# Kernel optimization log

Measured on AMD Instinct MI355X. Metric: run time of the kernel, lower is better.

Reference implementation:

```python
import jax, jax.numpy as jnp
import numpy as np
from jax import lax

DM = 64      # d_model
DI = 128     # d_inner = expand * d_model
DS = 16      # d_state
DC = 4       # d_conv
R = 4        # dt_rank = ceil(d_model/16)
H = 4        # num_heads
NL = 3       # num_mamba_stack
B_READS = 128
L_READ = 512
N_SEQ = 96


def setup_inputs() -> dict:
    key = jax.random.key(0)
    ks = jax.random.split(key, 20)
    f = lambda k, shape, s=0.05: jax.random.normal(k, shape, jnp.float32) * s
    A_init = jnp.broadcast_to(jnp.arange(1, DS + 1, dtype=jnp.float32), (NL, DI, DS))
    return {
        "reads": jax.random.normal(ks[0], (B_READS, L_READ, 4), jnp.float32),
        "sequenced_reads_indices": jax.random.randint(ks[1], (N_SEQ,), 0, B_READS),
        "expander_w": f(ks[2], (DM, 4), 0.3),
        "expander_b": f(ks[3], (DM,)),
        "in_proj_w": f(ks[4], (NL, 2 * DI, DM), 0.1),
        "conv_w": f(ks[5], (NL, DI, 1, DC), 0.3),
        "conv_b": f(ks[6], (NL, DI)),
        "x_proj_w": f(ks[7], (NL, R + 2 * DS, DI), 0.1),
        "dt_w": f(ks[8], (NL, DI, R), 0.3),
        "dt_b": f(ks[9], (NL, DI)),
        "A_log": jnp.log(A_init),
        "D": jnp.ones((NL, DI), jnp.float32),
        "out_w": f(ks[10], (NL, DM, DI), 0.1),
        "ln_w": jnp.ones((NL, DM), jnp.float32),
        "ln_b": jnp.zeros((NL, DM), jnp.float32),
        "query_w": f(ks[11], (DM, 2 * DM), 0.1),
        "query_b": f(ks[12], (DM,)),
        "key_w": f(ks[13], (DM, 2 * DM), 0.1),
        "key_b": f(ks[14], (DM,)),
        "mix_w": f(ks[15], (H, H), 0.3),
        "mix_b": f(ks[16], (H,)),
    }


def _mamba_block(u, in_w, cw, cb, xw, dtw, dtb, A_log, Dp, ow):
    # u: [b, l, DM]
    b, l, _ = u.shape
    xz = u @ in_w.T                              # [b, l, 2*DI]
    x, z = xz[..., :DI], xz[..., DI:]
    # causal depthwise conv along the sequence axis
    xc = lax.conv_general_dilated(
        x.transpose(0, 2, 1), cw, (1,), [(DC - 1, 0)],
        dimension_numbers=("NCH", "OIH", "NCH"), feature_group_count=DI)
    x = jax.nn.silu((xc + cb[None, :, None]).transpose(0, 2, 1))  # [b, l, DI]
    xd = x @ xw.T                                # [b, l, R + 2*DS]
    dt = jax.nn.softplus(xd[..., :R] @ dtw.T + dtb)              # [b, l, DI]
    Bm, Cm = xd[..., R:R + DS], xd[..., R + DS:]                 # [b, l, DS]
    A = -jnp.exp(A_log)                          # [DI, DS]

    def step(h, inp):
        x_t, dt_t, B_t, C_t = inp                # [b,DI],[b,DI],[b,DS],[b,DS]
        h = jnp.exp(dt_t[:, :, None] * A) * h + (dt_t * x_t)[:, :, None] * B_t[:, None, :]
        return h, jnp.einsum("bdn,bn->bd", h, C_t)

    h0 = jnp.zeros((b, DI, DS), u.dtype)
    _, ys = lax.scan(step, h0, (x.swapaxes(0, 1), dt.swapaxes(0, 1),
                                Bm.swapaxes(0, 1), Cm.swapaxes(0, 1)))
    y = ys.swapaxes(0, 1) + x * Dp               # [b, l, DI]
    y = y * jax.nn.silu(z)
    return y @ ow.T                              # [b, l, DM]


def _layer_norm(x, w, b, eps=1e-5):
    m = x.mean(-1, keepdims=True)
    v = ((x - m) ** 2).mean(-1, keepdims=True)
    return (x - m) / jnp.sqrt(v + eps) * w + b


def reference(reads, sequenced_reads_indices, expander_w, expander_b,
              in_proj_w, conv_w, conv_b, x_proj_w, dt_w, dt_b, A_log, D,
              out_w, ln_w, ln_b, query_w, query_b, key_w, key_b, mix_w, mix_b):
    h = reads @ expander_w.T + expander_b        # [b, l, DM]
    for i in range(NL):
        h = _mamba_block(h, in_proj_w[i], conv_w[i], conv_b[i], x_proj_w[i],
                         dt_w[i], dt_b[i], A_log[i], D[i], out_w[i])
        h = jax.nn.relu(_layer_norm(h, ln_w[i], ln_b[i]))
    mean_p = h.mean(1)                           # [b, DM]
    last_p = h[:, -1, :]                         # [b, DM]  (max_pooled in source is dead code)
    enc = jnp.concatenate([mean_p, last_p], axis=-1)   # [b, 2*DM]
    seq = enc[sequenced_reads_indices]                  # [q, 2*DM]
    q = (seq @ query_w.T + query_b).reshape(-1, H, DM // H).transpose(1, 0, 2)
    k = (enc @ key_w.T + key_b).reshape(-1, H, DM // H).transpose(1, 0, 2)
    scores = jnp.einsum("hqd,hkd->qkh", q, k)    # [q, b, H]
    scores = jax.nn.relu(scores) @ mix_w.T + mix_b
    return scores.max(-1)                        # [q, b]
```

## Files before the change

### kernel.cpp

```cpp
#include <hip/hip_runtime.h>
#include <hip/hip_bf16.h>
#include <math.h>

#define NLAYER 3
#define LREADx 512
#define NSEQx  96

typedef _Float16 f16x8 __attribute__((ext_vector_type(8)));
typedef _Float16 f16x4 __attribute__((ext_vector_type(4)));
typedef float    f32x4 __attribute__((ext_vector_type(4)));

__device__ __forceinline__ float fsigmoid(float v){ return 1.f/(1.f+__expf(-v)); }
__device__ __forceinline__ float fsoftplus(float v){ return fmaxf(v,0.f) + __logf(1.f + __expf(-fabsf(v))); }

__device__ __forceinline__ unsigned short f2h(float f){
  _Float16 h = (_Float16)f;
  return *reinterpret_cast<unsigned short*>(&h);
}

template<int CTRL>
__device__ __forceinline__ float dpp_add(float v){
  int x = __builtin_amdgcn_update_dpp(0, __float_as_int(v), CTRL, 0xF, 0xF, true);
  return v + __int_as_float(x);
}

__global__ __launch_bounds__(256) void k_exp(const float* __restrict__ reads,
    const float* __restrict__ ew, const float* __restrict__ eb, _Float16* __restrict__ h){
  int idx = blockIdx.x*256 + threadIdx.x;
  int dq = idx & 15;
  int row = idx >> 4;
  float4 r4 = *(const float4*)(reads + (size_t)row*4);
  f16x4 o;
  #pragma unroll
  for (int e=0;e<4;e++){
    int d = dq*4 + e;
    float4 w4 = *(const float4*)(ew + d*4);
    o[e] = (_Float16)fmaf(r4.x,w4.x, fmaf(r4.y,w4.y, fmaf(r4.z,w4.z, fmaf(r4.w,w4.w, eb[d]))));
  }
  *(f16x4*)(h + (size_t)row*64 + dq*4) = o;
}

__global__ __launch_bounds__(256) void k_wcvt(const float* __restrict__ inw,
    const float* __restrict__ ow, const float* __restrict__ xw,
    unsigned short* __restrict__ whf, unsigned short* __restrict__ owh,
    unsigned short* __restrict__ xwh){
  int i = blockIdx.x*256 + threadIdx.x;
  if (i < 49152){ whf[i] = f2h(inw[i]); return; }
  i -= 49152;
  if (i < 24576){ owh[i] = f2h(ow[i]); return; }
  i -= 24576;
  if (i < 18432){
    int l = i / 6144, rem = i % 6144;
    int r = rem >> 7, c = rem & 127;
    xwh[i] = (r < 36) ? f2h(xw[(l*36 + r)*128 + c]) : (unsigned short)0;
  }
}

__global__ __launch_bounds__(256) void k_xzc(const _Float16* __restrict__ h,
    const unsigned short* __restrict__ wb, const float* __restrict__ cw,
    const float* __restrict__ cb, _Float16* __restrict__ x, _Float16* __restrict__ zsil){
  __shared__ _Float16 hs_[80][68];
  __shared__ _Float16 xp[67][132];
  int t = threadIdx.x;
  int row0 = blockIdx.x*64;
  int l0 = row0 & 511;
  for (int i=t; i<640; i+=256){
    int r = i >> 3, q = i & 7;
    f16x8 v;
    #pragma unroll
    for (int e=0;e<8;e++) v[e] = (_Float16)0.f;
    if (!(l0==0 && r<16)) v = *(const f16x8*)(h + (size_t)(row0-16+r)*64 + q*8);
    *(f16x8*)&hs_[r][q*8] = v;
  }
  int w  = __builtin_amdgcn_readfirstlane(t >> 6);
  int ln = t & 63;
  int lr = ln & 15;
  int lk = (ln >> 4)*8;
  f16x8 bf[4][2];
  #pragma unroll
  for (int ct=0; ct<4; ct++)
    #pragma unroll
    for (int ks=0; ks<2; ks++)
      bf[ct][ks] = *(const f16x8*)(wb + (size_t)(w*64 + ct*16 + lr)*64 + ks*32 + lk);
  __syncthreads();
  f32x4 acc[5][4];
  #pragma unroll
  for (int m=0;m<5;m++)
    #pragma unroll
    for (int ct=0;ct<4;ct++) acc[m][ct] = (f32x4){0.f,0.f,0.f,0.f};
  #pragma unroll
  for (int m=0; m<5; m++){
    f16x8 a0 = *(const f16x8*)&hs_[m*16+lr][lk];
    f16x8 a1 = *(const f16x8*)&hs_[m*16+lr][32 + lk];
    #pragma unroll
    for (int ct=0; ct<4; ct++){
      acc[m][ct] = __builtin_amdgcn_mfma_f32_16x16x32_f16(a0, bf[ct][0], acc[m][ct], 0, 0, 0);
      acc[m][ct] = __builtin_amdgcn_mfma_f32_16x16x32_f16(a1, bf[ct][1], acc[m][ct], 0, 0, 0);
    }
  }
  int colb = w*64;
  #pragma unroll
  for (int m=0; m<5; m++)
    #pragma unroll
    for (int ct=0; ct<4; ct++){
      int col = colb + ct*16 + lr;
      #pragma unroll
      for (int rg=0; rg<4; rg++){
        int rl = m*16 + (ln>>4)*4 + rg;
        float v = acc[m][ct][rg];
        if (col < 128){
          if (rl >= 13) xp[rl-13][col] = (_Float16)v;
        } else {
          if (rl >= 16) zsil[(size_t)(row0 + rl - 16)*128 + (col-128)] = (_Float16)(v * fsigmoid(v));
        }
      }
    }
  __syncthreads();
  int c = t & 127, half = t >> 7;
  float4 w4 = *(const float4*)(cw + c*4);
  float bv = cb[c];
  #pragma unroll
  for (int r=half*32; r<half*32+32; r++){
    float a = fmaf((float)xp[r][c],w4.x, fmaf((float)xp[r+1][c],w4.y,
              fmaf((float)xp[r+2][c],w4.z, fmaf((float)xp[r+3][c],w4.w, bv))));
    x[(size_t)(row0+r)*128 + c] = (_Float16)(a * fsigmoid(a));
  }
}

__global__ __launch_bounds__(256) void k_xd(const _Float16* __restrict__ x,
    const unsigned short* __restrict__ xwh, const float* __restrict__ dtw,
    const float* __restrict__ dtb, float* __restrict__ dt, _Float16* __restrict__ bc){
  __shared__ _Float16 xst[64][136];
  __shared__ float xdl[64][37];
  int t = threadIdx.x;
  int row0 = blockIdx.x*64;
  for (int i=t; i<1024; i+=256){
    int r = i >> 4, q = i & 15;
    *(f16x8*)&xst[r][q*8] = *(const f16x8*)(x + (size_t)(row0+r)*128 + q*8);
  }
  __syncthreads();
  int w = __builtin_amdgcn_readfirstlane(t >> 6);
  int ln = t & 63, lr = ln & 15, kg = ln >> 4;
  f16x8 af[4];
  #pragma unroll
  for (int ks=0; ks<4; ks++) af[ks] = *(const f16x8*)&xst[w*16+lr][ks*32 + kg*8];
  f32x4 acc[3];
  #pragma unroll
  for (int ct=0;ct<3;ct++) acc[ct] = (f32x4){0.f,0.f,0.f,0.f};
  #pragma unroll
  for (int ks=0; ks<4; ks++)
    #pragma unroll
    for (int ct=0; ct<3; ct++){
      f16x8 b = *(const f16x8*)(xwh + (size_t)(ct*16 + lr)*128 + ks*32 + kg*8);
      acc[ct] = __builtin_amdgcn_mfma_f32_16x16x32_f16(af[ks], b, acc[ct], 0, 0, 0);
    }
  #pragma unroll
  for (int ct=0; ct<3; ct++){
    int c = ct*16 + lr;
    if (c < 36){
      #pragma unroll
      for (int rg=0; rg<4; rg++) xdl[w*16 + kg*4 + rg][c] = acc[ct][rg];
    }
  }
  __syncthreads();
  int d = t & 127, half = t >> 7;
  float4 w4 = *(const float4*)(dtw + d*4);
  float bv = dtb[d];
  size_t r0 = (size_t)blockIdx.x*64;
  for (int rr=half; rr<64; rr+=2){
    float v = fmaf(xdl[rr][0],w4.x, fmaf(xdl[rr][1],w4.y, fmaf(xdl[rr][2],w4.z,
              fmaf(xdl[rr][3],w4.w, bv))));
    dt[(r0+rr)*128 + d] = fsoftplus(v);
  }
  for (int i=t; i<2048; i+=256){
    int r = i >> 5, cc = i & 31;
    float vv = (cc & 1) ? xdl[r][20 + (cc>>1)] : xdl[r][4 + (cc>>1)];
    bc[(r0+r)*32 + cc] = (_Float16)vv;
  }
}

__global__ __launch_bounds__(256) void k_scan(const float* __restrict__ dt,
    const _Float16* __restrict__ x, const _Float16* __restrict__ zsil,
    const _Float16* __restrict__ bc, const float* __restrict__ alog,
    const float* __restrict__ Dp, _Float16* __restrict__ y){
  __shared__ float    dtxb[2][64*68];
  __shared__ _Float16 bcb [2][2048];
  __shared__ float    ys  [2][2048];
  int t = threadIdx.x;
  int b  = blockIdx.x & 127;
  int dg = blockIdx.x >> 7;
  int dl = t >> 3;
  int np = t & 7;
  int d  = dg*32 + dl;
  float aL1 = -__expf(alog[d*16 + 2*np])     * 1.44269504f;
  float aL2 = -__expf(alog[d*16 + 2*np + 1]) * 1.44269504f;
  float hs1 = 0.f, hs2 = 0.f;
  size_t base  = (size_t)b*512*128 + (size_t)dg*32;
  size_t baseb = (size_t)b*512*32;
  int r  = t >> 3;
  int d0 = (t & 7)*4;
  int rb = t >> 2;
  int cb_ = (t & 3)*8;
  const float*    dtA = dt   + base  + (size_t)r*128 + d0;
  const _Float16* xA  = x    + base  + (size_t)r*128 + d0;
  const _Float16* zA  = zsil + base  + (size_t)r*128 + d0;
  const _Float16* bA  = bc   + baseb + (size_t)rb*32 + cb_;
  float4 Dv4 = *(const float4*)(Dp + dg*32 + d0);

  auto stage = [&](int bsel, float4 pd0, float4 pd1, f16x4 px0, f16x4 px1, f16x8 pbh){
    float4 w0 = make_float4(pd0.x, pd0.x*(float)px0[0], pd0.y, pd0.y*(float)px0[1]);
    float4 w1 = make_float4(pd0.z, pd0.z*(float)px0[2], pd0.w, pd0.w*(float)px0[3]);
    float4 w2 = make_float4(pd1.x, pd1.x*(float)px1[0], pd1.y, pd1.y*(float)px1[1]);
    float4 w3 = make_float4(pd1.z, pd1.z*(float)px1[2], pd1.w, pd1.w*(float)px1[3]);
    *(float4*)&dtxb[bsel][r*68 + 2*d0]          = w0;
    *(float4*)&dtxb[bsel][r*68 + 2*d0 + 4]      = w1;
    *(float4*)&dtxb[bsel][(r+32)*68 + 2*d0]     = w2;
    *(float4*)&dtxb[bsel][(r+32)*68 + 2*d0 + 4] = w3;
    *(f16x8*)&bcb[bsel][rb*32 + cb_]            = pbh;
  };

  {
    float4 pd0 = *(const float4*)(dtA);
    float4 pd1 = *(const float4*)(dtA + 4096);
    f16x4  px0 = *(const f16x4*)(xA);
    f16x4  px1 = *(const f16x4*)(xA + 4096);
    f16x8  pbh = *(const f16x8*)(bA);
    stage(0, pd0, pd1, px0, px1, pbh);
  }
  asm volatile("s_waitcnt lgkmcnt(0)" ::: "memory");
  __builtin_amdgcn_s_barrier();

  for (int c=0;c<8;c++){
    int buf = c & 1;
    float4 nd0, nd1;
    f16x4  nx0, nx1;
    f16x8  nbh;
    if (c < 7){
      nd0 = *(const float4*)(dtA + (c+1)*8192);
      nd1 = *(const float4*)(dtA + (c+1)*8192 + 4096);
      nx0 = *(const f16x4*)(xA  + (c+1)*8192);
      nx1 = *(const f16x4*)(xA  + (c+1)*8192 + 4096);
      nbh = *(const f16x8*)(bA  + (c+1)*2048);
    }
    f16x4 xe0 = *(const f16x4*)(xA + c*8192);
    f16x4 xe1 = *(const f16x4*)(xA + c*8192 + 4096);
    f16x4 z0  = *(const f16x4*)(zA + c*8192);
    f16x4 z1  = *(const f16x4*)(zA + c*8192 + 4096);
    #pragma unroll 8
    for (int l=0;l<64;l++){
      float2 dx  = *(const float2*)&dtxb[buf][l*68 + 2*dl];
      f16x4 bch  = *(const f16x4*)&bcb[buf][l*32 + 4*np];
      float e1 = __builtin_amdgcn_exp2f(dx.x * aL1);
      float e2 = __builtin_amdgcn_exp2f(dx.x * aL2);
      hs1 = fmaf(e1, hs1, dx.y * (float)bch[0]);
      hs2 = fmaf(e2, hs2, dx.y * (float)bch[2]);
      float p = fmaf(hs1, (float)bch[1], hs2 * (float)bch[3]);
      p = dpp_add<0x101>(p);
      p = dpp_add<0x102>(p);
      p = dpp_add<0x104>(p);
      if (np == 0) ys[buf][l*32 + dl] = p;
    }
    if (c < 7) stage(buf^1, nd0, nd1, nx0, nx1, nbh);
    asm volatile("s_waitcnt lgkmcnt(0)" ::: "memory");
    __builtin_amdgcn_s_barrier();
    size_t yb = base + (size_t)c*8192;
    float4 s0 = *(const float4*)&ys[buf][4*t];
    float4 s1 = *(const float4*)&ys[buf][4*t + 1024];
    f16x4 o0, o1;
    o0[0] = (_Float16)((s0.x + (float)xe0[0]*Dv4.x) * (float)z0[0]);
    o0[1] = (_Float16)((s0.y + (float)xe0[1]*Dv4.y) * (float)z0[1]);
    o0[2] = (_Float16)((s0.z + (float)xe0[2]*Dv4.z) * (float)z0[2]);
    o0[3] = (_Float16)((s0.w + (float)xe0[3]*Dv4.w) * (float)z0[3]);
    o1[0] = (_Float16)((s1.x + (float)xe1[0]*Dv4.x) * (float)z1[0]);
    o1[1] = (_Float16)((s1.y + (float)xe1[1]*Dv4.y) * (float)z1[1]);
    o1[2] = (_Float16)((s1.z + (float)xe1[2]*Dv4.z) * (float)z1[2]);
    o1[3] = (_Float16)((s1.w + (float)xe1[3]*Dv4.w) * (float)z1[3]);
    *(f16x4*)(y + yb + (size_t)r*128 + d0)      = o0;
    *(f16x4*)(y + yb + (size_t)(r+32)*128 + d0) = o1;
  }
}

__global__ __launch_bounds__(256) void k_out(const _Float16* __restrict__ y,
    const unsigned short* __restrict__ owh, const float* __restrict__ lnw,
    const float* __restrict__ lnb, _Float16* __restrict__ h){
  __shared__ _Float16 yst[64][136];
  int t = threadIdx.x;
  int row0 = blockIdx.x*64;
  for (int i=t; i<1024; i+=256){
    int r = i >> 4, q = i & 15;
    *(f16x8*)&yst[r][q*8] = *(const f16x8*)(y + (size_t)(row0+r)*128 + q*8);
  }
  __syncthreads();
  int w = __builtin_amdgcn_readfirstlane(t >> 6);
  int ln = t & 63, lr = ln & 15, kg = ln >> 4;
  f16x8 af[4];
  #pragma unroll
  for (int ks=0; ks<4; ks++) af[ks] = *(const f16x8*)&yst[w*16+lr][ks*32 + kg*8];
  f32x4 acc[4];
  #pragma unroll
  for (int ct=0;ct<4;ct++) acc[ct] = (f32x4){0.f,0.f,0.f,0.f};
  #pragma unroll
  for (int ks=0; ks<4; ks++)
    #pragma unroll
    for (int ct=0; ct<4; ct++){
      f16x8 b = *(const f16x8*)(owh + (size_t)(ct*16 + lr)*128 + ks*32 + kg*8);
      acc[ct] = __builtin_amdgcn_mfma_f32_16x16x32_f16(af[ks], b, acc[ct], 0, 0, 0);
    }
  float mean[4], inv[4];
  #pragma unroll
  for (int rg=0; rg<4; rg++){
    float s = acc[0][rg] + acc[1][rg] + acc[2][rg] + acc[3][rg];
    #pragma unroll
    for (int off=1; off<16; off<<=1) s += __shfl_xor(s, off, 64);
    mean[rg] = s * (1.f/64.f);
  }
  #pragma unroll
  for (int rg=0; rg<4; rg++){
    float v = 0.f;
    #pragma unroll
    for (int ct=0; ct<4; ct++){ float dv = acc[ct][rg]-mean[rg]; v += dv*dv; }
    #pragma unroll
    for (int off=1; off<16; off<<=1) v += __shfl_xor(v, off, 64);
    inv[rg] = rsqrtf(v*(1.f/64.f) + 1e-5f);
  }
  float lw[4], lb[4];
  #pragma unroll
  for (int ct=0; ct<4; ct++){ lw[ct] = lnw[ct*16+lr]; lb[ct] = lnb[ct*16+lr]; }
  #pragma unroll
  for (int rg=0; rg<4; rg++){
    int row = row0 + w*16 + kg*4 + rg;
    #pragma unroll
    for (int ct=0; ct<4; ct++){
      float o = (acc[ct][rg]-mean[rg])*inv[rg]*lw[ct] + lb[ct];
      h[(size_t)row*64 + ct*16 + lr] = (_Float16)fmaxf(o, 0.f);
    }
  }
}

__global__ __launch_bounds__(512) void k_pool(const _Float16* __restrict__ h, float* __restrict__ enc){
  __shared__ float ps[8][64];
  int t = threadIdx.x;
  int w = t >> 6, d = t & 63;
  int b = blockIdx.x;
  const _Float16* hb = h + (size_t)b*LREADx*64;
  float s = 0.f;
  #pragma unroll 8
  for (int i=0;i<64;i++) s += (float)hb[(size_t)(w*64+i)*64 + d];
  ps[w][d] = s;
  __syncthreads();
  if (w == 0){
    float acc = 0.f;
    #pragma unroll
    for (int i=0;i<8;i++) acc += ps[i][d];
    enc[b*128 + d]      = acc * (1.f/512.f);
    enc[b*128 + 64 + d] = (float)hb[(size_t)511*64 + d];
  }
}

__global__ __launch_bounds__(256) void k_qk(const float* __restrict__ enc,
    const int* __restrict__ sidx, const float* __restrict__ qw, const float* __restrict__ qb,
    const float* __restrict__ kw, const float* __restrict__ kb,
    float* __restrict__ qbuf, float* __restrict__ kbuf){
  int idx = blockIdx.x*256 + threadIdx.x;
  if (idx < NSEQx*64){
    int qi = idx >> 6, j = idx & 63;
    const float* er = enc + (size_t)sidx[qi]*128;
    const float* wr = qw + j*128;
    float a = qb[j];
    for (int k=0;k<32;k++){
      float4 e4 = *(const float4*)(er + k*4);
      float4 w4 = *(const float4*)(wr + k*4);
      a = fmaf(e4.x,w4.x, fmaf(e4.y,w4.y, fmaf(e4.z,w4.z, fmaf(e4.w,w4.w, a))));
    }
    qbuf[idx] = a;
  } else {
    int i2 = idx - NSEQx*64;
    int ki = i2 >> 6, j = i2 & 63;
    const float* er = enc + (size_t)ki*128;
    const float* wr = kw + j*128;
    float a = kb[j];
    for (int k=0;k<32;k++){
      float4 e4 = *(const float4*)(er + k*4);
      float4 w4 = *(const float4*)(wr + k*4);
      a = fmaf(e4.x,w4.x, fmaf(e4.y,w4.y, fmaf(e4.z,w4.z, fmaf(e4.w,w4.w, a))));
    }
    kbuf[i2] = a;
  }
}

__global__ __launch_bounds__(256) void k_score(const float* __restrict__ qbuf,
    const float* __restrict__ kbuf, const float* __restrict__ mixw,
    const float* __restrict__ mixb, float* __restrict__ out){
  int idx = blockIdx.x*256 + threadIdx.x;
  int ki = idx & 127, qi = idx >> 7;
  const float* qr = qbuf + qi*64;
  const float* kr = kbuf + ki*64;
  float s[4];
  #pragma unroll
  for (int hh=0;hh<4;hh++){
    float a = 0.f;
    #pragma unroll
    for (int k=0;k<4;k++){
      float4 q4 = *(const float4*)(qr + hh*16 + k*4);
      float4 k4 = *(const float4*)(kr + hh*16 + k*4);
      a = fmaf(q4.x,k4.x, fmaf(q4.y,k4.y, fmaf(q4.z,k4.z, fmaf(q4.w,k4.w, a))));
    }
    s[hh] = fmaxf(a, 0.f);
  }
  float best = -1e30f;
  #pragma unroll
  for (int hh=0;hh<4;hh++){
    float v = mixb[hh];
    #pragma unroll
    for (int h2=0;h2<4;h2++) v = fmaf(s[h2], mixw[hh*4+h2], v);
    best = fmaxf(best, v);
  }
  out[idx] = best;
}

extern "C" void kernel_launch(void* const* d_in, const int* in_sizes, int n_in,
                              void* d_out, int out_size, void* d_ws, size_t ws_size,
                              hipStream_t stream) {
  (void)in_sizes; (void)n_in; (void)out_size; (void)ws_size;
  const float* reads = (const float*)d_in[0];
  const int*   sidx  = (const int*)d_in[1];
  const float* ew    = (const float*)d_in[2];
  const float* eb    = (const float*)d_in[3];
  const float* inw   = (const float*)d_in[4];
  const float* cw    = (const float*)d_in[5];
  const float* cb    = (const float*)d_in[6];
  const float* xw    = (const float*)d_in[7];
  const float* dtw   = (const float*)d_in[8];
  const float* dtb   = (const float*)d_in[9];
  const float* alog  = (const float*)d_in[10];
  const float* Dp    = (const float*)d_in[11];
  const float* ow    = (const float*)d_in[12];
  const float* lnw   = (const float*)d_in[13];
  const float* lnb   = (const float*)d_in[14];
  const float* qw    = (const float*)d_in[15];
  const float* qb    = (const float*)d_in[16];
  const float* kw    = (const float*)d_in[17];
  const float* kb    = (const float*)d_in[18];
  const float* mixw  = (const float*)d_in[19];
  const float* mixb  = (const float*)d_in[20];

  float* ws  = (float*)d_ws;
  _Float16* h  = (_Float16*)(ws);
  _Float16* yx = (_Float16*)(ws + 4194304);
  _Float16* zs = (_Float16*)(ws + 12582912);
  _Float16* x  = (_Float16*)(ws + 20971520);
  float* dt  = ws + 29360128;
  _Float16* bc = (_Float16*)(ws + 37748736);
  float* enc = ws + 39845888;
  float* qk  = ws + 39862272;
  unsigned short* whf = (unsigned short*)(ws + 39876608);
  unsigned short* owh = whf + 49152;
  unsigned short* xwh = owh + 24576;

  k_wcvt <<<360, 256, 0, stream>>>(inw, ow, xw, whf, owh, xwh);
  k_exp  <<<4096, 256, 0, stream>>>(reads, ew, eb, h);
  for (int l = 0; l < NLAYER; l++){
    k_xzc <<<1024, 256, 0, stream>>>(h, whf + l*16384, cw + l*512, cb + l*128, x, zs);
    k_xd  <<<1024, 256, 0, stream>>>(x, xwh + l*6144, dtw + l*512, dtb + l*128, dt, bc);
    k_scan<<<512, 256, 0, stream>>>(dt, x, zs, bc, alog + l*2048, Dp + l*128, yx);
    k_out <<<1024, 256, 0, stream>>>(yx, owh + l*8192, lnw + l*64, lnb + l*64, h);
  }
  k_pool <<<128, 512, 0, stream>>>(h, enc);
  k_qk   <<<56, 256, 0, stream>>>(enc, sidx, qw, qb, kw, kb, qk, qk + 6144);
  k_score<<<48, 256, 0, stream>>>(qk, qk + 6144, mixw, mixb, (float*)d_out);
}
```

Before: 368.0 us.

## Split scan work to one state per thread and double scan block count

The selective scan kernel now gives each thread a single state element (16 threads per channel) instead of two, and each block handles 16 channels instead of 32, so the grid doubles from 512 to 1024 blocks. The serial dependency chain per thread is halved, at the cost of one extra DPP reduction step and more blocks each re-staging the shared B/C data. Shared memory per block shrinks, which may allow higher occupancy.

```diff
diff --git a/kernel.cpp b/kernel.cpp
--- a/kernel.cpp
+++ b/kernel.cpp
@@ -8,6 +8,7 @@
 
 typedef _Float16 f16x8 __attribute__((ext_vector_type(8)));
 typedef _Float16 f16x4 __attribute__((ext_vector_type(4)));
+typedef _Float16 f16x2 __attribute__((ext_vector_type(2)));
 typedef float    f32x4 __attribute__((ext_vector_type(4)));
 
 __device__ __forceinline__ float fsigmoid(float v){ return 1.f/(1.f+__expf(-v)); }
@@ -183,100 +184,80 @@
     const _Float16* __restrict__ x, const _Float16* __restrict__ zsil,
     const _Float16* __restrict__ bc, const float* __restrict__ alog,
     const float* __restrict__ Dp, _Float16* __restrict__ y){
-  __shared__ float    dtxb[2][64*68];
+  __shared__ float    dtxb[2][64*36];
   __shared__ _Float16 bcb [2][2048];
-  __shared__ float    ys  [2][2048];
+  __shared__ float    ys  [2][1024];
   int t = threadIdx.x;
   int b  = blockIdx.x & 127;
   int dg = blockIdx.x >> 7;
-  int dl = t >> 3;
-  int np = t & 7;
-  int d  = dg*32 + dl;
-  float aL1 = -__expf(alog[d*16 + 2*np])     * 1.44269504f;
-  float aL2 = -__expf(alog[d*16 + 2*np + 1]) * 1.44269504f;
-  float hs1 = 0.f, hs2 = 0.f;
-  size_t base  = (size_t)b*512*128 + (size_t)dg*32;
+  int dl = t >> 4;
+  int n  = t & 15;
+  int d  = dg*16 + dl;
+  float aL = -__expf(alog[d*16 + n]) * 1.44269504f;
+  float hs = 0.f;
+  size_t base  = (size_t)b*512*128 + (size_t)dg*16;
   size_t baseb = (size_t)b*512*32;
-  int r  = t >> 3;
-  int d0 = (t & 7)*4;
-  int rb = t >> 2;
-  int cb_ = (t & 3)*8;
-  const float*    dtA = dt   + base  + (size_t)r*128 + d0;
-  const _Float16* xA  = x    + base  + (size_t)r*128 + d0;
-  const _Float16* zA  = zsil + base  + (size_t)r*128 + d0;
-  const _Float16* bA  = bc   + baseb + (size_t)rb*32 + cb_;
-  float4 Dv4 = *(const float4*)(Dp + dg*32 + d0);
-
-  auto stage = [&](int bsel, float4 pd0, float4 pd1, f16x4 px0, f16x4 px1, f16x8 pbh){
-    float4 w0 = make_float4(pd0.x, pd0.x*(float)px0[0], pd0.y, pd0.y*(float)px0[1]);
-    float4 w1 = make_float4(pd0.z, pd0.z*(float)px0[2], pd0.w, pd0.w*(float)px0[3]);
-    float4 w2 = make_float4(pd1.x, pd1.x*(float)px1[0], pd1.y, pd1.y*(float)px1[1]);
-    float4 w3 = make_float4(pd1.z, pd1.z*(float)px1[2], pd1.w, pd1.w*(float)px1[3]);
-    *(float4*)&dtxb[bsel][r*68 + 2*d0]          = w0;
-    *(float4*)&dtxb[bsel][r*68 + 2*d0 + 4]      = w1;
-    *(float4*)&dtxb[bsel][(r+32)*68 + 2*d0]     = w2;
-    *(float4*)&dtxb[bsel][(r+32)*68 + 2*d0 + 4] = w3;
-    *(f16x8*)&bcb[bsel][rb*32 + cb_]            = pbh;
+  int ls = t >> 2;
+  int q  = t & 3;
+  const float*    dtA = dt   + base  + (size_t)ls*128 + q*4;
+  const _Float16* xA  = x    + base  + (size_t)ls*128 + q*4;
+  const _Float16* zA  = zsil + base  + (size_t)ls*128 + q*4;
+  const _Float16* bA  = bc   + baseb + (size_t)ls*32  + q*8;
+  float4 Dv4 = *(const float4*)(Dp + dg*16 + q*4);
+
+  auto stage = [&](int bsel, float4 pd, f16x4 px, f16x8 pbh){
+    float4 w0 = make_float4(pd.x, pd.x*(float)px[0], pd.y, pd.y*(float)px[1]);
+    float4 w1 = make_float4(pd.z, pd.z*(float)px[2], pd.w, pd.w*(float)px[3]);
+    *(float4*)&dtxb[bsel][ls*36 + 8*q]     = w0;
+    *(float4*)&dtxb[bsel][ls*36 + 8*q + 4] = w1;
+    *(f16x8*)&bcb[bsel][ls*32 + q*8]       = pbh;
   };
 
   {
-    float4 pd0 = *(const float4*)(dtA);
-    float4 pd1 = *(const float4*)(dtA + 4096);
-    f16x4  px0 = *(const f16x4*)(xA);
-    f16x4  px1 = *(const f16x4*)(xA + 4096);
+    float4 pd = *(const float4*)(dtA);
+    f16x4  px = *(const f16x4*)(xA);
     f16x8  pbh = *(const f16x8*)(bA);
-    stage(0, pd0, pd1, px0, px1, pbh);
+    stage(0, pd, px, pbh);
   }
   asm volatile("s_waitcnt lgkmcnt(0)" ::: "memory");
   __builtin_amdgcn_s_barrier();
 
   for (int c=0;c<8;c++){
     int buf = c & 1;
-    float4 nd0, nd1;
-    f16x4  nx0, nx1;
+    float4 nd;
+    f16x4  nx;
     f16x8  nbh;
     if (c < 7){
-      nd0 = *(const float4*)(dtA + (c+1)*8192);
-      nd1 = *(const float4*)(dtA + (c+1)*8192 + 4096);
-      nx0 = *(const f16x4*)(xA  + (c+1)*8192);
-      nx1 = *(const f16x4*)(xA  + (c+1)*8192 + 4096);
+      nd  = *(const float4*)(dtA + (c+1)*8192);
+      nx  = *(const f16x4*)(xA  + (c+1)*8192);
       nbh = *(const f16x8*)(bA  + (c+1)*2048);
     }
-    f16x4 xe0 = *(const f16x4*)(xA + c*8192);
-    f16x4 xe1 = *(const f16x4*)(xA + c*8192 + 4096);
-    f16x4 z0  = *(const f16x4*)(zA + c*8192);
-    f16x4 z1  = *(const f16x4*)(zA + c*8192 + 4096);
+    f16x4 xe = *(const f16x4*)(xA + c*8192);
+    f16x4 ze = *(const f16x4*)(zA + c*8192);
     #pragma unroll 8
     for (int l=0;l<64;l++){
-      float2 dx  = *(const float2*)&dtxb[buf][l*68 + 2*dl];
-      f16x4 bch  = *(const f16x4*)&bcb[buf][l*32 + 4*np];
-      float e1 = __builtin_amdgcn_exp2f(dx.x * aL1);
-      float e2 = __builtin_amdgcn_exp2f(dx.x * aL2);
-      hs1 = fmaf(e1, hs1, dx.y * (float)bch[0]);
-      hs2 = fmaf(e2, hs2, dx.y * (float)bch[2]);
-      float p = fmaf(hs1, (float)bch[1], hs2 * (float)bch[3]);
+      float2 dx = *(const float2*)&dtxb[buf][l*36 + 2*dl];
+      f16x2 bch = *(const f16x2*)&bcb[buf][l*32 + 2*n];
+      float e = __builtin_amdgcn_exp2f(dx.x * aL);
+      hs = fmaf(e, hs, dx.y * (float)bch[0]);
+      float p = hs * (float)bch[1];
       p = dpp_add<0x101>(p);
       p = dpp_add<0x102>(p);
       p = dpp_add<0x104>(p);
-      if (np == 0) ys[buf][l*32 + dl] = p;
-    }
-    if (c < 7) stage(buf^1, nd0, nd1, nx0, nx1, nbh);
+      p = dpp_add<0x108>(p);
+      if (n == 0) ys[buf][l*16 + dl] = p;
+    }
+    if (c < 7) stage(buf^1, nd, nx, nbh);
     asm volatile("s_waitcnt lgkmcnt(0)" ::: "memory");
     __builtin_amdgcn_s_barrier();
     size_t yb = base + (size_t)c*8192;
-    float4 s0 = *(const float4*)&ys[buf][4*t];
-    float4 s1 = *(const float4*)&ys[buf][4*t + 1024];
-    f16x4 o0, o1;
-    o0[0] = (_Float16)((s0.x + (float)xe0[0]*Dv4.x) * (float)z0[0]);
-    o0[1] = (_Float16)((s0.y + (float)xe0[1]*Dv4.y) * (float)z0[1]);
-    o0[2] = (_Float16)((s0.z + (float)xe0[2]*Dv4.z) * (float)z0[2]);
-    o0[3] = (_Float16)((s0.w + (float)xe0[3]*Dv4.w) * (float)z0[3]);
-    o1[0] = (_Float16)((s1.x + (float)xe1[0]*Dv4.x) * (float)z1[0]);
-    o1[1] = (_Float16)((s1.y + (float)xe1[1]*Dv4.y) * (float)z1[1]);
-    o1[2] = (_Float16)((s1.z + (float)xe1[2]*Dv4.z) * (float)z1[2]);
-    o1[3] = (_Float16)((s1.w + (float)xe1[3]*Dv4.w) * (float)z1[3]);
-    *(f16x4*)(y + yb + (size_t)r*128 + d0)      = o0;
-    *(f16x4*)(y + yb + (size_t)(r+32)*128 + d0) = o1;
+    float4 s = *(const float4*)&ys[buf][ls*16 + q*4];
+    f16x4 o;
+    o[0] = (_Float16)((s.x + (float)xe[0]*Dv4.x) * (float)ze[0]);
+    o[1] = (_Float16)((s.y + (float)xe[1]*Dv4.y) * (float)ze[1]);
+    o[2] = (_Float16)((s.z + (float)xe[2]*Dv4.z) * (float)ze[2]);
+    o[3] = (_Float16)((s.w + (float)xe[3]*Dv4.w) * (float)ze[3]);
+    *(f16x4*)(y + yb + (size_t)ls*128 + q*4) = o;
   }
 }
 
@@ -462,7 +443,7 @@
   for (int l = 0; l < NLAYER; l++){
     k_xzc <<<1024, 256, 0, stream>>>(h, whf + l*16384, cw + l*512, cb + l*128, x, zs);
     k_xd  <<<1024, 256, 0, stream>>>(x, xwh + l*6144, dtw + l*512, dtb + l*128, dt, bc);
-    k_scan<<<512, 256, 0, stream>>>(dt, x, zs, bc, alog + l*2048, Dp + l*128, yx);
+    k_scan<<<1024, 256, 0, stream>>>(dt, x, zs, bc, alog + l*2048, Dp + l*128, yx);
     k_out <<<1024, 256, 0, stream>>>(yx, owh + l*8192, lnw + l*64, lnb + l*64, h);
   }
   k_pool <<<128, 512, 0, stream>>>(h, enc);
```

Measured after the change: 403.9 us. 9.8% more time.
